# Optimization experiments

Hardware: AMD Instinct MI355X
Metric: run time of the kernel (lower is better)

Reference implementation:

```python
import jax, jax.numpy as jnp
import numpy as np

N_ATOMS = 100000
N_BONDS = 200001
ATOM_FDIM = 39
BOND_FDIM = 11
MAX_NB = 6
HIDDEN = 256
DEPTH = 6
N_MOLS = 2000
ATOMS_PER_MOL = N_ATOMS // N_MOLS


def setup_inputs() -> dict:
    key = jax.random.key(0)
    ks = jax.random.split(key, 8)
    fatoms = jax.random.uniform(ks[0], (N_ATOMS, ATOM_FDIM), dtype=jnp.float32)
    fbonds = jax.random.uniform(ks[1], (N_BONDS, ATOM_FDIM + BOND_FDIM), dtype=jnp.float32)
    agraph = jax.random.randint(ks[2], (N_ATOMS, MAX_NB), 0, N_BONDS, dtype=jnp.int32)
    bgraph = jax.random.randint(ks[3], (N_BONDS, MAX_NB), 0, N_BONDS, dtype=jnp.int32)
    starts = jnp.arange(N_MOLS, dtype=jnp.int32) * ATOMS_PER_MOL
    scope = jnp.stack([starts, jnp.full((N_MOLS,), ATOMS_PER_MOL, jnp.int32)], axis=1)
    s = 1.0 / np.sqrt(HIDDEN)
    W_i = jax.random.normal(ks[4], (HIDDEN, ATOM_FDIM + BOND_FDIM), dtype=jnp.float32) * s
    W_h = jax.random.normal(ks[5], (HIDDEN, HIDDEN), dtype=jnp.float32) * s
    W_o = jax.random.normal(ks[6], (HIDDEN, ATOM_FDIM + HIDDEN), dtype=jnp.float32) * s
    b_o = jax.random.normal(ks[7], (HIDDEN,), dtype=jnp.float32) * s
    return {"fatoms": fatoms, "fbonds": fbonds, "agraph": agraph,
            "bgraph": bgraph, "scope": scope, "W_i": W_i, "W_h": W_h,
            "W_o": W_o, "b_o": b_o}


def reference(fatoms, fbonds, agraph, bgraph, scope, W_i, W_h, W_o, b_o):
    # Initial bond messages: Linear (no bias) + ReLU
    binput = fbonds @ W_i.T                      # [B_bonds, H]
    message = jax.nn.relu(binput)
    # depth-1 rounds of gather -> sum over MAX_NB neighbors -> Linear -> ReLU + residual
    for _ in range(DEPTH - 1):
        nei = message[bgraph].sum(axis=1)        # [B_bonds, H]
        message = jax.nn.relu(binput + nei @ W_h.T)
    # Atom readout
    nei = message[agraph].sum(axis=1)            # [N_atoms, H]
    ainput = jnp.concatenate([fatoms, nei], axis=1)
    atom_hiddens = jax.nn.relu(ainput @ W_o.T + b_o)
    # Scope mean pooling: equal-size contiguous segments -> reshape-mean
    n_mols = scope.shape[0]
    mol_vecs = atom_hiddens.reshape(n_mols, -1, atom_hiddens.shape[-1]).mean(axis=1)
    return mol_vecs
```

## Files before the change

kernel.cpp:

```cpp
#include <hip/hip_runtime.h>
#include <hip/hip_bf16.h>

#define NB 200001
#define NA 100000
#define HID 256
#define AF 39
#define BFD 50
#define MAXNB 6
#define NMOL 2000
#define APM 50
#define KPAD 320

typedef __attribute__((ext_vector_type(8))) unsigned short ushort8;
typedef __attribute__((ext_vector_type(8))) short short8;
typedef __attribute__((ext_vector_type(4))) float f32x4;

__device__ __forceinline__ unsigned short f2b(float f) {
  __hip_bfloat16 h = __float2bfloat16(f);
  return *reinterpret_cast<unsigned short*>(&h);
}
__device__ __forceinline__ float b2f(unsigned short u) {
  union { unsigned int i; float f; } v; v.i = ((unsigned int)u) << 16; return v.f;
}

__global__ void prep_wc(const float* __restrict__ Wi, const float* __restrict__ Wh,
                        unsigned short* __restrict__ WcB) {
  int i = blockIdx.x * 256 + threadIdx.x;
  if (i >= HID * KPAD) return;
  int n = i / KPAD, k = i % KPAD;
  float v = 0.f;
  if (k < BFD) v = Wi[n * BFD + k];
  else if (k >= 64) v = Wh[n * HID + (k - 64)];
  WcB[i] = f2b(v);
}
__global__ void prep_wo(const float* __restrict__ Wo, unsigned short* __restrict__ WoP) {
  int i = blockIdx.x * 256 + threadIdx.x;
  if (i >= HID * KPAD) return;
  int n = i / KPAD, k = i % KPAD;
  float v = 0.f;
  if (k < AF) v = Wo[n * (AF + HID) + k];
  else if (k >= 64) v = Wo[n * (AF + HID) + AF + (k - 64)];
  WoP[i] = f2b(v);
}

__global__ __launch_bounds__(256, 2) void init_kernel(
    const float* __restrict__ fbonds, const unsigned short* __restrict__ WcB,
    unsigned short* __restrict__ msg0) {
  __shared__ unsigned short As[64][64];
  __shared__ unsigned short Bs[256][64];
  const int t = threadIdx.x;
  const int b0 = blockIdx.x * 64;

  {
    const int rs = t >> 3, csl = t & 7;
    #pragma unroll
    for (int it = 0; it < 2; ++it) {
      const int r = it * 32 + rs;
      const int bond = b0 + r;
      const int c0 = csl * 8;
      ushort8 o;
      #pragma unroll
      for (int e = 0; e < 8; ++e) {
        const int c = c0 + e;
        float v = (bond < NB && c < BFD) ? fbonds[(size_t)bond * BFD + c] : 0.f;
        o[e] = f2b(v);
      }
      *reinterpret_cast<ushort8*>(&As[r][c0 ^ ((r & 7) << 3)]) = o;
    }
  }
  {
    #pragma unroll
    for (int i = 0; i < 8; ++i) {
      const int idx = i * 256 + t;
      const int n = idx >> 3;
      const int c0 = (idx & 7) * 8;
      ushort8 v = *reinterpret_cast<const ushort8*>(WcB + (size_t)n * KPAD + c0);
      *reinterpret_cast<ushort8*>(&Bs[n][c0 ^ ((n & 7) << 3)]) = v;
    }
  }
  __syncthreads();

  const int w = t >> 6, lane = t & 63, lr = lane & 15, lg = lane >> 4;
  f32x4 acc[4][4];
  #pragma unroll
  for (int i = 0; i < 4; ++i)
    #pragma unroll
    for (int j = 0; j < 4; ++j) acc[i][j] = f32x4{0.f, 0.f, 0.f, 0.f};

  #pragma unroll
  for (int ks = 0; ks < 2; ++ks) {
    const int kb = ks * 32 + lg * 8;
    short8 a[4], b[4];
    #pragma unroll
    for (int fm = 0; fm < 4; ++fm) {
      const int m = fm * 16 + lr;
      a[fm] = *reinterpret_cast<const short8*>(&As[m][kb ^ ((m & 7) << 3)]);
    }
    #pragma unroll
    for (int fn = 0; fn < 4; ++fn) {
      const int n = w * 64 + fn * 16 + lr;
      b[fn] = *reinterpret_cast<const short8*>(&Bs[n][kb ^ ((n & 7) << 3)]);
    }
    #pragma unroll
    for (int fm = 0; fm < 4; ++fm)
      #pragma unroll
      for (int fn = 0; fn < 4; ++fn)
        acc[fm][fn] = __builtin_amdgcn_mfma_f32_16x16x32_bf16(a[fm], b[fn], acc[fm][fn], 0, 0, 0);
  }

  #pragma unroll
  for (int fm = 0; fm < 4; ++fm)
    #pragma unroll
    for (int r = 0; r < 4; ++r) {
      const int m = fm * 16 + lg * 4 + r;
      const int bond = b0 + m;
      if (bond < NB) {
        #pragma unroll
        for (int fn = 0; fn < 4; ++fn) {
          const int col = w * 64 + fn * 16 + lr;
          msg0[(size_t)bond * HID + col] = f2b(fmaxf(acc[fm][fn][r], 0.f));
        }
      }
    }
}

__global__ __launch_bounds__(256, 2) void round_kernel(
    const unsigned short* __restrict__ msg_in, unsigned short* __restrict__ msg_out,
    const float* __restrict__ fbonds, const unsigned short* __restrict__ WcB,
    const int* __restrict__ bgraph) {
  __shared__ unsigned short As[64][KPAD];
  __shared__ unsigned short Bs[256][64];
  const int t = threadIdx.x;
  const int b0 = blockIdx.x * 64;

  {
    const int rs = t >> 3, csl = t & 7;
    #pragma unroll
    for (int it = 0; it < 2; ++it) {
      const int r = it * 32 + rs;
      const int bond = b0 + r;
      const int c0 = csl * 8;
      ushort8 o;
      #pragma unroll
      for (int e = 0; e < 8; ++e) {
        const int c = c0 + e;
        float v = (bond < NB && c < BFD) ? fbonds[(size_t)bond * BFD + c] : 0.f;
        o[e] = f2b(v);
      }
      *reinterpret_cast<ushort8*>(&As[r][c0 ^ ((r & 7) << 3)]) = o;
    }
  }
  {
    const int rslot = t >> 5;
    const int c0 = (t & 31) * 8;
    #pragma unroll
    for (int it = 0; it < 8; ++it) {
      const int r = it * 8 + rslot;
      const int bond = b0 + r;
      float acc[8] = {0.f, 0.f, 0.f, 0.f, 0.f, 0.f, 0.f, 0.f};
      if (bond < NB) {
        const int* bg = bgraph + (size_t)bond * MAXNB;
        #pragma unroll
        for (int j = 0; j < MAXNB; ++j) {
          const int nb = bg[j];
          ushort8 v = *reinterpret_cast<const ushort8*>(msg_in + (size_t)nb * HID + c0);
          #pragma unroll
          for (int e = 0; e < 8; ++e) acc[e] += b2f(v[e]);
        }
      }
      ushort8 o;
      #pragma unroll
      for (int e = 0; e < 8; ++e) o[e] = f2b(acc[e]);
      const int cc = 64 + c0;
      *reinterpret_cast<ushort8*>(&As[r][cc ^ ((r & 7) << 3)]) = o;
    }
  }

  const int w = t >> 6, lane = t & 63, lr = lane & 15, lg = lane >> 4;
  f32x4 acc[4][4];
  #pragma unroll
  for (int i = 0; i < 4; ++i)
    #pragma unroll
    for (int j = 0; j < 4; ++j) acc[i][j] = f32x4{0.f, 0.f, 0.f, 0.f};

  for (int kstep = 0; kstep < 5; ++kstep) {
    __syncthreads();
    {
      #pragma unroll
      for (int i = 0; i < 8; ++i) {
        const int idx = i * 256 + t;
        const int n = idx >> 3;
        const int c0 = (idx & 7) * 8;
        ushort8 v = *reinterpret_cast<const ushort8*>(WcB + (size_t)n * KPAD + kstep * 64 + c0);
        *reinterpret_cast<ushort8*>(&Bs[n][c0 ^ ((n & 7) << 3)]) = v;
      }
    }
    __syncthreads();
    #pragma unroll
    for (int ks = 0; ks < 2; ++ks) {
      const int kb = ks * 32 + lg * 8;
      const int kA = kstep * 64 + kb;
      short8 a[4], b[4];
      #pragma unroll
      for (int fm = 0; fm < 4; ++fm) {
        const int m = fm * 16 + lr;
        a[fm] = *reinterpret_cast<const short8*>(&As[m][kA ^ ((m & 7) << 3)]);
      }
      #pragma unroll
      for (int fn = 0; fn < 4; ++fn) {
        const int n = w * 64 + fn * 16 + lr;
        b[fn] = *reinterpret_cast<const short8*>(&Bs[n][kb ^ ((n & 7) << 3)]);
      }
      #pragma unroll
      for (int fm = 0; fm < 4; ++fm)
        #pragma unroll
        for (int fn = 0; fn < 4; ++fn)
          acc[fm][fn] = __builtin_amdgcn_mfma_f32_16x16x32_bf16(a[fm], b[fn], acc[fm][fn], 0, 0, 0);
    }
  }

  #pragma unroll
  for (int fm = 0; fm < 4; ++fm)
    #pragma unroll
    for (int r = 0; r < 4; ++r) {
      const int m = fm * 16 + lg * 4 + r;
      const int bond = b0 + m;
      if (bond < NB) {
        #pragma unroll
        for (int fn = 0; fn < 4; ++fn) {
          const int col = w * 64 + fn * 16 + lr;
          msg_out[(size_t)bond * HID + col] = f2b(fmaxf(acc[fm][fn][r], 0.f));
        }
      }
    }
}

__global__ __launch_bounds__(256, 2) void readout_kernel(
    const unsigned short* __restrict__ msg_in, const float* __restrict__ fatoms,
    const unsigned short* __restrict__ WoP, const float* __restrict__ b_o,
    const int* __restrict__ agraph, float* __restrict__ atomh) {
  __shared__ unsigned short As[64][KPAD];
  __shared__ unsigned short Bs[256][64];
  const int t = threadIdx.x;
  const int a0 = blockIdx.x * 64;

  {
    const int rs = t >> 3, csl = t & 7;
    #pragma unroll
    for (int it = 0; it < 2; ++it) {
      const int r = it * 32 + rs;
      const int atom = a0 + r;
      const int c0 = csl * 8;
      ushort8 o;
      #pragma unroll
      for (int e = 0; e < 8; ++e) {
        const int c = c0 + e;
        float v = (atom < NA && c < AF) ? fatoms[(size_t)atom * AF + c] : 0.f;
        o[e] = f2b(v);
      }
      *reinterpret_cast<ushort8*>(&As[r][c0 ^ ((r & 7) << 3)]) = o;
    }
  }
  {
    const int rslot = t >> 5;
    const int c0 = (t & 31) * 8;
    #pragma unroll
    for (int it = 0; it < 8; ++it) {
      const int r = it * 8 + rslot;
      const int atom = a0 + r;
      float acc[8] = {0.f, 0.f, 0.f, 0.f, 0.f, 0.f, 0.f, 0.f};
      if (atom < NA) {
        const int* ag = agraph + (size_t)atom * MAXNB;
        #pragma unroll
        for (int j = 0; j < MAXNB; ++j) {
          const int nb = ag[j];
          ushort8 v = *reinterpret_cast<const ushort8*>(msg_in + (size_t)nb * HID + c0);
          #pragma unroll
          for (int e = 0; e < 8; ++e) acc[e] += b2f(v[e]);
        }
      }
      ushort8 o;
      #pragma unroll
      for (int e = 0; e < 8; ++e) o[e] = f2b(acc[e]);
      const int cc = 64 + c0;
      *reinterpret_cast<ushort8*>(&As[r][cc ^ ((r & 7) << 3)]) = o;
    }
  }

  const int w = t >> 6, lane = t & 63, lr = lane & 15, lg = lane >> 4;
  f32x4 acc[4][4];
  #pragma unroll
  for (int i = 0; i < 4; ++i)
    #pragma unroll
    for (int j = 0; j < 4; ++j) acc[i][j] = f32x4{0.f, 0.f, 0.f, 0.f};

  for (int kstep = 0; kstep < 5; ++kstep) {
    __syncthreads();
    {
      #pragma unroll
      for (int i = 0; i < 8; ++i) {
        const int idx = i * 256 + t;
        const int n = idx >> 3;
        const int c0 = (idx & 7) * 8;
        ushort8 v = *reinterpret_cast<const ushort8*>(WoP + (size_t)n * KPAD + kstep * 64 + c0);
        *reinterpret_cast<ushort8*>(&Bs[n][c0 ^ ((n & 7) << 3)]) = v;
      }
    }
    __syncthreads();
    #pragma unroll
    for (int ks = 0; ks < 2; ++ks) {
      const int kb = ks * 32 + lg * 8;
      const int kA = kstep * 64 + kb;
      short8 a[4], b[4];
      #pragma unroll
      for (int fm = 0; fm < 4; ++fm) {
        const int m = fm * 16 + lr;
        a[fm] = *reinterpret_cast<const short8*>(&As[m][kA ^ ((m & 7) << 3)]);
      }
      #pragma unroll
      for (int fn = 0; fn < 4; ++fn) {
        const int n = w * 64 + fn * 16 + lr;
        b[fn] = *reinterpret_cast<const short8*>(&Bs[n][kb ^ ((n & 7) << 3)]);
      }
      #pragma unroll
      for (int fm = 0; fm < 4; ++fm)
        #pragma unroll
        for (int fn = 0; fn < 4; ++fn)
          acc[fm][fn] = __builtin_amdgcn_mfma_f32_16x16x32_bf16(a[fm], b[fn], acc[fm][fn], 0, 0, 0);
    }
  }

  #pragma unroll
  for (int fm = 0; fm < 4; ++fm)
    #pragma unroll
    for (int r = 0; r < 4; ++r) {
      const int m = fm * 16 + lg * 4 + r;
      const int atom = a0 + m;
      if (atom < NA) {
        #pragma unroll
        for (int fn = 0; fn < 4; ++fn) {
          const int col = w * 64 + fn * 16 + lr;
          const float v = acc[fm][fn][r] + b_o[col];
          atomh[(size_t)atom * HID + col] = fmaxf(v, 0.f);
        }
      }
    }
}

__global__ __launch_bounds__(256) void pool_kernel(const float* __restrict__ atomh,
                                                   float* __restrict__ out) {
  const int mol = blockIdx.x;
  const int t = threadIdx.x;
  const float* base = atomh + (size_t)mol * APM * HID + t;
  float s = 0.f;
  #pragma unroll 5
  for (int i = 0; i < APM; ++i) s += base[(size_t)i * HID];
  out[(size_t)mol * HID + t] = s * (1.f / APM);
}

extern "C" void kernel_launch(void* const* d_in, const int* in_sizes, int n_in,
                              void* d_out, int out_size, void* d_ws, size_t ws_size,
                              hipStream_t stream) {
  const float* fatoms = (const float*)d_in[0];
  const float* fbonds = (const float*)d_in[1];
  const int* agraph = (const int*)d_in[2];
  const int* bgraph = (const int*)d_in[3];
  const float* W_i = (const float*)d_in[5];
  const float* W_h = (const float*)d_in[6];
  const float* W_o = (const float*)d_in[7];
  const float* b_o = (const float*)d_in[8];

  char* ws = (char*)d_ws;
  size_t off = 0;
  auto alloc = [&](size_t bytes) {
    void* p = ws + off;
    off += (bytes + 255) & ~(size_t)255;
    return p;
  };
  unsigned short* msgA = (unsigned short*)alloc((size_t)NB * HID * 2);
  unsigned short* msgB = (unsigned short*)alloc((size_t)NB * HID * 2);
  unsigned short* WcB = (unsigned short*)alloc((size_t)HID * KPAD * 2);
  unsigned short* WoP = (unsigned short*)alloc((size_t)HID * KPAD * 2);
  float* atomh = (float*)msgA;

  if (ws_size < off) return;

  prep_wc<<<(HID * KPAD + 255) / 256, 256, 0, stream>>>(W_i, W_h, WcB);
  prep_wo<<<(HID * KPAD + 255) / 256, 256, 0, stream>>>(W_o, WoP);

  const int nblk_b = (NB + 63) / 64;
  init_kernel<<<nblk_b, 256, 0, stream>>>(fbonds, WcB, msgA);

  unsigned short* src = msgA;
  unsigned short* dst = msgB;
  for (int d = 0; d < 5; ++d) {
    round_kernel<<<nblk_b, 256, 0, stream>>>(src, dst, fbonds, WcB, bgraph);
    unsigned short* tmp = src; src = dst; dst = tmp;
  }

  const int nblk_a = (NA + 63) / 64;
  readout_kernel<<<nblk_a, 256, 0, stream>>>(src, fatoms, WoP, b_o, agraph, atomh);
  pool_kernel<<<NMOL, 256, 0, stream>>>(atomh, (float*)d_out);
}
```

Baseline: 0.9996 ms.

## Read weight fragments directly from global, drop LDS B staging, prepad bond features

```diff
diff --git a/kernel.cpp b/kernel.cpp
--- a/kernel.cpp
+++ b/kernel.cpp
@@ -42,42 +42,56 @@
   else if (k >= 64) v = Wo[n * (AF + HID) + AF + (k - 64)];
   WoP[i] = f2b(v);
 }
-
-__global__ __launch_bounds__(256, 2) void init_kernel(
-    const float* __restrict__ fbonds, const unsigned short* __restrict__ WcB,
-    unsigned short* __restrict__ msg0) {
-  __shared__ unsigned short As[64][64];
-  __shared__ unsigned short Bs[256][64];
+__global__ void prep_fb(const float* __restrict__ fbonds, unsigned short* __restrict__ fbpad) {
+  int i = blockIdx.x * 256 + threadIdx.x;
+  if (i >= NB * 8) return;
+  const int bond = i >> 3;
+  const int c0 = (i & 7) * 8;
+  ushort8 o;
+  #pragma unroll
+  for (int e = 0; e < 8; ++e) {
+    const int c = c0 + e;
+    o[e] = f2b(c < BFD ? fbonds[(size_t)bond * BFD + c] : 0.f);
+  }
+  *reinterpret_cast<ushort8*>(fbpad + (size_t)bond * 64 + c0) = o;
+}
+
+template <bool PREPPED>
+__device__ __forceinline__ void stage_feat64(unsigned short (*As)[KPAD], int t, int b0,
+                                             int nrows_total,
+                                             const float* __restrict__ f32src, int f32dim, int realdim,
+                                             const unsigned short* __restrict__ padsrc) {
+  const int rs = t >> 3, csl = t & 7;
+  #pragma unroll
+  for (int it = 0; it < 2; ++it) {
+    const int r = it * 32 + rs;
+    const int row = b0 + r;
+    const int c0 = csl * 8;
+    ushort8 o;
+    #pragma unroll
+    for (int e = 0; e < 8; ++e) o[e] = 0;
+    if (PREPPED) {
+      if (row < nrows_total) o = *reinterpret_cast<const ushort8*>(padsrc + (size_t)row * 64 + c0);
+    } else {
+      #pragma unroll
+      for (int e = 0; e < 8; ++e) {
+        const int c = c0 + e;
+        if (row < nrows_total && c < realdim) o[e] = f2b(f32src[(size_t)row * f32dim + c]);
+      }
+    }
+    *reinterpret_cast<ushort8*>(&As[r][c0 ^ ((r & 7) << 3)]) = o;
+  }
+}
+
+template <bool PREPPED>
+__global__ __launch_bounds__(256, 4) void init_kernel(
+    const float* __restrict__ fbonds, const unsigned short* __restrict__ fbpad,
+    const unsigned short* __restrict__ WcB, unsigned short* __restrict__ msg0) {
+  __shared__ unsigned short As[64][KPAD];
   const int t = threadIdx.x;
   const int b0 = blockIdx.x * 64;
 
-  {
-    const int rs = t >> 3, csl = t & 7;
-    #pragma unroll
-    for (int it = 0; it < 2; ++it) {
-      const int r = it * 32 + rs;
-      const int bond = b0 + r;
-      const int c0 = csl * 8;
-      ushort8 o;
-      #pragma unroll
-      for (int e = 0; e < 8; ++e) {
-        const int c = c0 + e;
-        float v = (bond < NB && c < BFD) ? fbonds[(size_t)bond * BFD + c] : 0.f;
-        o[e] = f2b(v);
-      }
-      *reinterpret_cast<ushort8*>(&As[r][c0 ^ ((r & 7) << 3)]) = o;
-    }
-  }
-  {
-    #pragma unroll
-    for (int i = 0; i < 8; ++i) {
-      const int idx = i * 256 + t;
-      const int n = idx >> 3;
-      const int c0 = (idx & 7) * 8;
-      ushort8 v = *reinterpret_cast<const ushort8*>(WcB + (size_t)n * KPAD + c0);
-      *reinterpret_cast<ushort8*>(&Bs[n][c0 ^ ((n & 7) << 3)]) = v;
-    }
-  }
+  stage_feat64<PREPPED>(As, t, b0, NB, fbonds, BFD, BFD, fbpad);
   __syncthreads();
 
   const int w = t >> 6, lane = t & 63, lr = lane & 15, lg = lane >> 4;
@@ -86,6 +100,10 @@
   for (int i = 0; i < 4; ++i)
     #pragma unroll
     for (int j = 0; j < 4; ++j) acc[i][j] = f32x4{0.f, 0.f, 0.f, 0.f};
+
+  const unsigned short* wb[4];
+  #pragma unroll
+  for (int fn = 0; fn < 4; ++fn) wb[fn] = WcB + (size_t)(w * 64 + fn * 16 + lr) * KPAD;
 
   #pragma unroll
   for (int ks = 0; ks < 2; ++ks) {
@@ -97,10 +115,8 @@
       a[fm] = *reinterpret_cast<const short8*>(&As[m][kb ^ ((m & 7) << 3)]);
     }
     #pragma unroll
-    for (int fn = 0; fn < 4; ++fn) {
-      const int n = w * 64 + fn * 16 + lr;
-      b[fn] = *reinterpret_cast<const short8*>(&Bs[n][kb ^ ((n & 7) << 3)]);
-    }
+    for (int fn = 0; fn < 4; ++fn)
+      b[fn] = *reinterpret_cast<const short8*>(wb[fn] + kb);
     #pragma unroll
     for (int fm = 0; fm < 4; ++fm)
       #pragma unroll
@@ -124,32 +140,17 @@
     }
 }
 
-__global__ __launch_bounds__(256, 2) void round_kernel(
+template <bool PREPPED>
+__global__ __launch_bounds__(256, 4) void round_kernel(
     const unsigned short* __restrict__ msg_in, unsigned short* __restrict__ msg_out,
-    const float* __restrict__ fbonds, const unsigned short* __restrict__ WcB,
-    const int* __restrict__ bgraph) {
+    const float* __restrict__ fbonds, const unsigned short* __restrict__ fbpad,
+    const unsigned short* __restrict__ WcB, const int* __restrict__ bgraph) {
   __shared__ unsigned short As[64][KPAD];
-  __shared__ unsigned short Bs[256][64];
   const int t = threadIdx.x;
   const int b0 = blockIdx.x * 64;
 
-  {
-    const int rs = t >> 3, csl = t & 7;
-    #pragma unroll
-    for (int it = 0; it < 2; ++it) {
-      const int r = it * 32 + rs;
-      const int bond = b0 + r;
-      const int c0 = csl * 8;
-      ushort8 o;
-      #pragma unroll
-      for (int e = 0; e < 8; ++e) {
-        const int c = c0 + e;
-        float v = (bond < NB && c < BFD) ? fbonds[(size_t)bond * BFD + c] : 0.f;
-        o[e] = f2b(v);
-      }
-      *reinterpret_cast<ushort8*>(&As[r][c0 ^ ((r & 7) << 3)]) = o;
-    }
-  }
+  stage_feat64<PREPPED>(As, t, b0, NB, fbonds, BFD, BFD, fbpad);
+
   {
     const int rslot = t >> 5;
     const int c0 = (t & 31) * 8;
@@ -175,6 +176,7 @@
       *reinterpret_cast<ushort8*>(&As[r][cc ^ ((r & 7) << 3)]) = o;
     }
   }
+  __syncthreads();
 
   const int w = t >> 6, lane = t & 63, lr = lane & 15, lg = lane >> 4;
   f32x4 acc[4][4];
@@ -183,19 +185,11 @@
     #pragma unroll
     for (int j = 0; j < 4; ++j) acc[i][j] = f32x4{0.f, 0.f, 0.f, 0.f};
 
+  const unsigned short* wb[4];
+  #pragma unroll
+  for (int fn = 0; fn < 4; ++fn) wb[fn] = WcB + (size_t)(w * 64 + fn * 16 + lr) * KPAD;
+
   for (int kstep = 0; kstep < 5; ++kstep) {
-    __syncthreads();
-    {
-      #pragma unroll
-      for (int i = 0; i < 8; ++i) {
-        const int idx = i * 256 + t;
-        const int n = idx >> 3;
-        const int c0 = (idx & 7) * 8;
-        ushort8 v = *reinterpret_cast<const ushort8*>(WcB + (size_t)n * KPAD + kstep * 64 + c0);
-        *reinterpret_cast<ushort8*>(&Bs[n][c0 ^ ((n & 7) << 3)]) = v;
-      }
-    }
-    __syncthreads();
     #pragma unroll
     for (int ks = 0; ks < 2; ++ks) {
       const int kb = ks * 32 + lg * 8;
@@ -207,10 +201,8 @@
         a[fm] = *reinterpret_cast<const short8*>(&As[m][kA ^ ((m & 7) << 3)]);
       }
       #pragma unroll
-      for (int fn = 0; fn < 4; ++fn) {
-        const int n = w * 64 + fn * 16 + lr;
-        b[fn] = *reinterpret_cast<const short8*>(&Bs[n][kb ^ ((n & 7) << 3)]);
-      }
+      for (int fn = 0; fn < 4; ++fn)
+        b[fn] = *reinterpret_cast<const short8*>(wb[fn] + kstep * 64 + kb);
       #pragma unroll
       for (int fm = 0; fm < 4; ++fm)
         #pragma unroll
@@ -235,32 +227,16 @@
     }
 }
 
-__global__ __launch_bounds__(256, 2) void readout_kernel(
+__global__ __launch_bounds__(256, 4) void readout_kernel(
     const unsigned short* __restrict__ msg_in, const float* __restrict__ fatoms,
     const unsigned short* __restrict__ WoP, const float* __restrict__ b_o,
     const int* __restrict__ agraph, float* __restrict__ atomh) {
   __shared__ unsigned short As[64][KPAD];
-  __shared__ unsigned short Bs[256][64];
   const int t = threadIdx.x;
   const int a0 = blockIdx.x * 64;
 
-  {
-    const int rs = t >> 3, csl = t & 7;
-    #pragma unroll
-    for (int it = 0; it < 2; ++it) {
-      const int r = it * 32 + rs;
-      const int atom = a0 + r;
-      const int c0 = csl * 8;
-      ushort8 o;
-      #pragma unroll
-      for (int e = 0; e < 8; ++e) {
-        const int c = c0 + e;
-        float v = (atom < NA && c < AF) ? fatoms[(size_t)atom * AF + c] : 0.f;
-        o[e] = f2b(v);
-      }
-      *reinterpret_cast<ushort8*>(&As[r][c0 ^ ((r & 7) << 3)]) = o;
-    }
-  }
+  stage_feat64<false>(As, t, a0, NA, fatoms, AF, AF, nullptr);
+
   {
     const int rslot = t >> 5;
     const int c0 = (t & 31) * 8;
@@ -286,6 +262,7 @@
       *reinterpret_cast<ushort8*>(&As[r][cc ^ ((r & 7) << 3)]) = o;
     }
   }
+  __syncthreads();
 
   const int w = t >> 6, lane = t & 63, lr = lane & 15, lg = lane >> 4;
   f32x4 acc[4][4];
@@ -294,19 +271,11 @@
     #pragma unroll
     for (int j = 0; j < 4; ++j) acc[i][j] = f32x4{0.f, 0.f, 0.f, 0.f};
 
+  const unsigned short* wb[4];
+  #pragma unroll
+  for (int fn = 0; fn < 4; ++fn) wb[fn] = WoP + (size_t)(w * 64 + fn * 16 + lr) * KPAD;
+
   for (int kstep = 0; kstep < 5; ++kstep) {
-    __syncthreads();
-    {
-      #pragma unroll
-      for (int i = 0; i < 8; ++i) {
-        const int idx = i * 256 + t;
-        const int n = idx >> 3;
-        const int c0 = (idx & 7) * 8;
-        ushort8 v = *reinterpret_cast<const ushort8*>(WoP + (size_t)n * KPAD + kstep * 64 + c0);
-        *reinterpret_cast<ushort8*>(&Bs[n][c0 ^ ((n & 7) << 3)]) = v;
-      }
-    }
-    __syncthreads();
     #pragma unroll
     for (int ks = 0; ks < 2; ++ks) {
       const int kb = ks * 32 + lg * 8;
@@ -318,10 +287,8 @@
         a[fm] = *reinterpret_cast<const short8*>(&As[m][kA ^ ((m & 7) << 3)]);
       }
       #pragma unroll
-      for (int fn = 0; fn < 4; ++fn) {
-        const int n = w * 64 + fn * 16 + lr;
-        b[fn] = *reinterpret_cast<const short8*>(&Bs[n][kb ^ ((n & 7) << 3)]);
-      }
+      for (int fn = 0; fn < 4; ++fn)
+        b[fn] = *reinterpret_cast<const short8*>(wb[fn] + kstep * 64 + kb);
       #pragma unroll
       for (int fm = 0; fm < 4; ++fm)
         #pragma unroll
@@ -381,20 +348,32 @@
   unsigned short* msgB = (unsigned short*)alloc((size_t)NB * HID * 2);
   unsigned short* WcB = (unsigned short*)alloc((size_t)HID * KPAD * 2);
   unsigned short* WoP = (unsigned short*)alloc((size_t)HID * KPAD * 2);
+  const size_t base_need = off;
+  unsigned short* fbpad = (unsigned short*)alloc((size_t)NB * 64 * 2);
+  const size_t fb_need = off;
   float* atomh = (float*)msgA;
 
-  if (ws_size < off) return;
+  if (ws_size < base_need) return;
+  const bool prepped = (ws_size >= fb_need);
 
   prep_wc<<<(HID * KPAD + 255) / 256, 256, 0, stream>>>(W_i, W_h, WcB);
   prep_wo<<<(HID * KPAD + 255) / 256, 256, 0, stream>>>(W_o, WoP);
+  if (prepped)
+    prep_fb<<<(NB * 8 + 255) / 256, 256, 0, stream>>>(fbonds, fbpad);
 
   const int nblk_b = (NB + 63) / 64;
-  init_kernel<<<nblk_b, 256, 0, stream>>>(fbonds, WcB, msgA);
+  if (prepped)
+    init_kernel<true><<<nblk_b, 256, 0, stream>>>(fbonds, fbpad, WcB, msgA);
+  else
+    init_kernel<false><<<nblk_b, 256, 0, stream>>>(fbonds, fbpad, WcB, msgA);
 
   unsigned short* src = msgA;
   unsigned short* dst = msgB;
   for (int d = 0; d < 5; ++d) {
-    round_kernel<<<nblk_b, 256, 0, stream>>>(src, dst, fbonds, WcB, bgraph);
+    if (prepped)
+      round_kernel<true><<<nblk_b, 256, 0, stream>>>(src, dst, fbonds, fbpad, WcB, bgraph);
+    else
+      round_kernel<false><<<nblk_b, 256, 0, stream>>>(src, dst, fbonds, fbpad, WcB, bgraph);
     unsigned short* tmp = src; src = dst; dst = tmp;
   }
 
```

New measurement: 946.3 us. -5.3%, faster.
